# Kernel tuning notes

Hardware: AMD Instinct MI355X
Metric: run time of the kernel (lower is better)

## Reference

```python
import jax, jax.numpy as jnp
from jax import lax
import numpy as np

LEVELS = 5
KSIZE = 45
SIGMA0 = 1.0
SIZE_ADDER = 0
SIGMA_MULT = 2.0


def _gauss1d(ksize, sigma):
    # Matches cv2.getGaussianKernel for sigma > 0: normalized Gaussian samples.
    x = np.arange(ksize, dtype=np.float64) - (ksize - 1) / 2.0
    g = np.exp(-(x * x) / (2.0 * sigma * sigma))
    return g / g.sum()


def _gauss2d(ksize, sigma):
    g1 = _gauss1d(ksize, sigma)
    return jnp.asarray(np.outer(g1, g1), dtype=jnp.float32)  # (k, k)


_KERNELS = [_gauss2d(KSIZE + SIZE_ADDER, SIGMA0 * SIGMA_MULT ** lvl) for lvl in range(LEVELS)]


def _blur(img, k2d):
    """Depthwise 2D Gaussian blur with replicate padding. img: (N,C,H,W), k2d: (k,k)."""
    C = img.shape[1]
    k = k2d.shape[0]
    pad = k // 2
    imgp = jnp.pad(img, ((0, 0), (0, 0), (pad, pad), (pad, pad)), mode='edge')
    kern = jnp.broadcast_to(k2d.astype(img.dtype), (C, 1, k, k))  # same filter per channel
    return lax.conv_general_dilated(
        imgp, kern, window_strides=(1, 1), padding='VALID',
        dimension_numbers=('NCHW', 'OIHW', 'NCHW'), feature_group_count=C)


def _blend(img0, img1, mask):
    # Fused Laplacian-stack build for img0/img1, Gaussian-stack for mask, and
    # lerp + sum-over-levels accumulation in a single pass over levels.
    cur0, cur1, curm = img0, img1, mask
    acc = jnp.zeros_like(img0)
    for lvl in range(LEVELS):
        if lvl < LEVELS - 1:
            k2d = _KERNELS[lvl]
            b0 = _blur(cur0, k2d)
            b1 = _blur(cur1, k2d)
            bm = _blur(curm, k2d)
            lap0 = cur0 - b0
            lap1 = cur1 - b1
            acc = acc + lap0 + curm * (lap1 - lap0)  # lerp(lap0, lap1, gauss_mask)
            cur0, cur1, curm = b0, b1, bm
        else:
            acc = acc + cur0 + curm * (cur1 - cur0)
    return acc


def setup_inputs() -> dict:
    key = jax.random.key(0)
    k0, k1, k2 = jax.random.split(key, 3)
    img0 = jax.random.normal(k0, (16, 3, 512, 512), dtype=jnp.float32)
    img1 = jax.random.normal(k1, (16, 3, 512, 512), dtype=jnp.float32)
    mask = jax.random.uniform(k2, (16, 1, 512, 512), dtype=jnp.float32)
    return {"img0": img0, "img1": img1, "mask": mask}


def reference(img0, img1, mask):
    return _blend(img0, img1, mask)
```

## Files before the change

### kernel.cpp

```cpp
#include <hip/hip_runtime.h>

#define PH 512
#define PW 512
#define PLANE (PH * PW)
#define RS 68
#define PHYS(i) (((i) & 7) * 70 + ((i) >> 3))

enum { V_F0 = 0, V_MID = 1, V_L3D = 2, V_MONLY = 3 };

constexpr double cexp_pos(double z) {
  double term = 1.0, sum = 1.0;
  for (int k = 1; k < 160; ++k) {
    term *= z / (double)k;
    sum += term;
  }
  return sum;
}
template <int LVL, int R>
struct WTab {
  float w[2 * R + 1];
  constexpr WTab() : w{} {
    double sig = 1.0;
    for (int i = 0; i < LVL; ++i) sig *= 2.0;
    double g[2 * R + 1] = {};
    double s = 0.0;
    for (int t = 0; t <= 2 * R; ++t) {
      double x = (double)(t - R);
      g[t] = 1.0 / cexp_pos((x * x) / (2.0 * sig * sig));
      s += g[t];
    }
    for (int t = 0; t <= 2 * R; ++t) w[t] = (float)(g[t] / s);
  }
};

__device__ __forceinline__ int clampi(int v, int hi) {
  return v < 0 ? 0 : (v > hi ? hi : v);
}
__device__ __forceinline__ int swz(int bid, int nwg) {
  const int q = nwg >> 3;
  return (bid & 7) * q + (bid >> 3);
}
__device__ __forceinline__ float bf2f(ushort s) {
  return __uint_as_float((unsigned)s << 16);
}
__device__ __forceinline__ ushort f2bf(float f) {
  unsigned x = __float_as_uint(f);
  return (ushort)((x + 0x7FFF + ((x >> 16) & 1)) >> 16);
}
union BU { uint4 q; ushort u[8]; };
__device__ __forceinline__ void ldb8(const ushort* __restrict__ p, float* v) {
  BU b;
  b.q = *(const uint4*)p;
#pragma unroll
  for (int j = 0; j < 8; ++j) v[j] = bf2f(b.u[j]);
}
__device__ __forceinline__ void stb8(ushort* __restrict__ p, const float* v) {
  BU b;
#pragma unroll
  for (int j = 0; j < 8; ++j) b.u[j] = f2bf(v[j]);
  *(uint4*)p = b.q;
}
__device__ __forceinline__ void ldf8(const float* __restrict__ p, float* v) {
  float4 a = *(const float4*)p, b = *(const float4*)(p + 4);
  v[0] = a.x; v[1] = a.y; v[2] = a.z; v[3] = a.w;
  v[4] = b.x; v[5] = b.y; v[6] = b.z; v[7] = b.w;
}
__device__ __forceinline__ void stf8(float* __restrict__ p, const float* v) {
  *(float4*)p = make_float4(v[0], v[1], v[2], v[3]);
  *(float4*)(p + 4) = make_float4(v[4], v[5], v[6], v[7]);
}

template <int LVL, int R, bool LV0>
__global__ __launch_bounds__(256) void hpass_tele(
    const ushort* __restrict__ S, const float* __restrict__ in0,
    const float* __restrict__ in1, const float* __restrict__ inm,
    ushort* __restrict__ tmp, int cn3) {
  constexpr WTab<LVL, R> W;
  const int bid = swz(blockIdx.x, gridDim.x);
  const int tid = threadIdx.x;
  const int ry = tid >> 6, lr = tid & 63;
  const int p = bid >> 7;
  const int y = ((bid & 127) << 2) + ry;
  const int xb = lr << 3;

  __shared__ float lds[4][8 * 70];
  float* L = lds[ry];

  if (LV0) {
    if (p < cn3) {
      const float* rA = in0 + (size_t)p * PLANE + (size_t)y * PW;
      const float* rB = in1 + (size_t)p * PLANE + (size_t)y * PW;
      float a8[8], b8[8];
      ldf8(rA + xb, a8);
      ldf8(rB + xb, b8);
#pragma unroll
      for (int k = 0; k < 8; ++k) L[PHYS(R + xb + k)] = b8[k] - a8[k];
      if (lr < R) L[PHYS(lr)] = rB[0] - rA[0];
      else if (lr >= 32 && lr < 32 + R)
        L[PHYS(R + PW + (lr - 32))] = rB[PW - 1] - rA[PW - 1];
    } else {
      const float* rM = inm + (size_t)(p - cn3) * PLANE + (size_t)y * PW;
      float a8[8];
      ldf8(rM + xb, a8);
#pragma unroll
      for (int k = 0; k < 8; ++k) L[PHYS(R + xb + k)] = a8[k];
      if (lr < R) L[PHYS(lr)] = rM[0];
      else if (lr >= 32 && lr < 32 + R)
        L[PHYS(R + PW + (lr - 32))] = rM[PW - 1];
    }
  } else {
    const ushort* row = S + (size_t)p * PLANE + (size_t)y * PW;
    float a8[8];
    ldb8(row + xb, a8);
#pragma unroll
    for (int k = 0; k < 8; ++k) L[PHYS(R + xb + k)] = a8[k];
    if (lr < R) L[PHYS(lr)] = bf2f(row[0]);
    else if (lr >= 32 && lr < 32 + R)
      L[PHYS(R + PW + (lr - 32))] = bf2f(row[PW - 1]);
  }
  __syncthreads();

  float a[8];
#pragma unroll
  for (int i = 0; i < 8; ++i) a[i] = 0.f;
#pragma unroll
  for (int j = 0; j < 2 * R + 8; ++j) {
    const float v = L[PHYS(xb + j)];
#pragma unroll
    for (int i = 0; i < 8; ++i)
      if (i <= j && j - i <= 2 * R) a[i] = fmaf(W.w[j - i], v, a[i]);
  }
  stb8(tmp + (size_t)p * PLANE + (size_t)y * PW + xb, a);
}

template <int LVL, int R, int MODE>
__global__ __launch_bounds__(512) void vpass_tele(
    const ushort* __restrict__ tmp, const ushort* __restrict__ Sc,
    const ushort* __restrict__ Sm, const ushort* __restrict__ Gm4,
    const float* __restrict__ in0, const float* __restrict__ in1,
    const float* __restrict__ inm, ushort* __restrict__ oS,
    ushort* __restrict__ oM, float* __restrict__ outp, int cn3) {
  constexpr WTab<LVL, R> W;
  constexpr int VWIN = 64 + 2 * R;
  __shared__ float buf[VWIN * RS];
  const int bid = swz(blockIdx.x, gridDim.x);
  const int tid = threadIdx.x;
  const int lane = tid & 63, yg = tid >> 6;
  const int p = bid >> 6, t = bid & 63;
  const int x0 = (t & 7) << 6, y0 = (t >> 3) << 6;
  const int ey = tid >> 3, exq = (tid & 7) << 3;
  const size_t erow = (size_t)(y0 + ey) * PW + x0 + exq;

  const bool ismask = (MODE == V_MONLY) || (MODE != V_L3D && p >= cn3);
  const int pm = ismask ? ((MODE == V_MONLY) ? p : p - cn3) : 0;

  {
    const ushort* src = tmp + (size_t)(ismask ? (cn3 + pm) : p) * PLANE;
    for (int idx = tid; idx < VWIN * 8; idx += 512) {
      const int row = idx >> 3, c8 = (idx & 7) << 3;
      const int gy = clampi(y0 + row - R, PH - 1);
      BU b;
      b.q = *(const uint4*)&src[(size_t)gy * PW + x0 + c8];
      float* d = &buf[row * RS + c8];
#pragma unroll
      for (int j = 0; j < 8; ++j) d[j] = bf2f(b.u[j]);
    }
  }
  __syncthreads();

  float b[8];
#pragma unroll
  for (int i = 0; i < 8; ++i) b[i] = 0.f;
#pragma unroll
  for (int j = 0; j < 2 * R + 8; ++j) {
    const float v = buf[((yg << 3) + j) * RS + lane];
#pragma unroll
    for (int i = 0; i < 8; ++i)
      if (i <= j && j - i <= 2 * R) b[i] = fmaf(W.w[j - i], v, b[i]);
  }

  __syncthreads();
#pragma unroll
  for (int i = 0; i < 8; ++i) buf[lane * 65 + (yg << 3) + i] = b[i];
  __syncthreads();
  float bs[8];
#pragma unroll
  for (int j = 0; j < 8; ++j) bs[j] = buf[(exq + j) * 65 + ey];

  if (MODE == V_MONLY || ismask) {
    stb8(oM + (size_t)pm * PLANE + erow, bs);
    return;
  }

  const int n = p / 3;
  float o[8];
  if (MODE == V_F0) {
    float v0[8], v1[8], m[8];
    ldf8(in0 + (size_t)p * PLANE + erow, v0);
    ldf8(in1 + (size_t)p * PLANE + erow, v1);
    ldf8(inm + (size_t)n * PLANE + erow, m);
#pragma unroll
    for (int j = 0; j < 8; ++j)
      o[j] = v0[j] + m[j] * ((v1[j] - v0[j]) - bs[j]);
    stf8(outp + (size_t)p * PLANE + erow, o);
    stb8(oS + (size_t)p * PLANE + erow, bs);
  } else if (MODE == V_MID) {
    float D[8], m[8], pv[8];
    ldb8(Sc + (size_t)p * PLANE + erow, D);
    ldb8(Sm + (size_t)n * PLANE + erow, m);
    float* op = outp + (size_t)p * PLANE + erow;
    ldf8(op, pv);
#pragma unroll
    for (int j = 0; j < 8; ++j) o[j] = pv[j] + m[j] * (D[j] - bs[j]);
    stf8(op, o);
    stb8(oS + (size_t)p * PLANE + erow, bs);
  } else {
    float D[8], m3[8], m4[8], pv[8];
    ldb8(Sc + (size_t)p * PLANE + erow, D);
    ldb8(Sm + (size_t)n * PLANE + erow, m3);
    ldb8(Gm4 + (size_t)n * PLANE + erow, m4);
    float* op = outp + (size_t)p * PLANE + erow;
    ldf8(op, pv);
#pragma unroll
    for (int j = 0; j < 8; ++j)
      o[j] = pv[j] + m3[j] * (D[j] - bs[j]) + m4[j] * bs[j];
    stf8(op, o);
  }
}

extern "C" void kernel_launch(void* const* d_in, const int* in_sizes, int n_in,
                              void* d_out, int out_size, void* d_ws,
                              size_t ws_size, hipStream_t stream) {
  const float* img0 = (const float*)d_in[0];
  const float* img1 = (const float*)d_in[1];
  const float* mask = (const float*)d_in[2];
  float* out = (float*)d_out;

  constexpr int R0 = 6, R1 = 10, R2 = 18, R3v = 22;

  const int NTOT = 16;
  const size_t perImg = (size_t)12 * PLANE * sizeof(ushort);
  int CN = 16;
  while (CN > 1 && (size_t)CN * perImg > ws_size) CN >>= 1;

  for (int s = 0; s < NTOT; s += CN) {
    ushort* SA = (ushort*)d_ws;
    ushort* SB = SA + (size_t)4 * CN * PLANE;
    ushort* tmp = SB + (size_t)4 * CN * PLANE;

    const float* in0 = img0 + (size_t)s * 3 * PLANE;
    const float* in1 = img1 + (size_t)s * 3 * PLANE;
    const float* inm = mask + (size_t)s * PLANE;
    float* o = out + (size_t)s * 3 * PLANE;

    const int cn3 = 3 * CN;
    ushort* SAm = SA + (size_t)cn3 * PLANE;
    ushort* SBm = SB + (size_t)cn3 * PLANE;
    const ushort* nb = nullptr;
    const float* nf = nullptr;
    const dim3 hb(256), vb(512);
    const int hg = 4 * CN * 128;
    const int vg = 4 * CN * 64;
    const int vgM = CN * 64;
    const int vgD = 3 * CN * 64;

    hipLaunchKernelGGL((hpass_tele<0, R0, true>), dim3(hg), hb, 0, stream, nb,
                       in0, in1, inm, tmp, cn3);
    hipLaunchKernelGGL((vpass_tele<0, R0, V_F0>), dim3(vg), vb, 0, stream, tmp,
                       nb, nb, nb, in0, in1, inm, SA, SAm, o, cn3);
    hipLaunchKernelGGL((hpass_tele<1, R1, false>), dim3(hg), hb, 0, stream, SA,
                       nf, nf, nf, tmp, cn3);
    hipLaunchKernelGGL((vpass_tele<1, R1, V_MID>), dim3(vg), vb, 0, stream, tmp,
                       SA, SAm, nb, nf, nf, nf, SB, SBm, o, cn3);
    hipLaunchKernelGGL((hpass_tele<2, R2, false>), dim3(hg), hb, 0, stream, SB,
                       nf, nf, nf, tmp, cn3);
    hipLaunchKernelGGL((vpass_tele<2, R2, V_MID>), dim3(vg), vb, 0, stream, tmp,
                       SB, SBm, nb, nf, nf, nf, SA, SAm, o, cn3);
    hipLaunchKernelGGL((hpass_tele<3, R3v, false>), dim3(hg), hb, 0, stream, SA,
                       nf, nf, nf, tmp, cn3);
    hipLaunchKernelGGL((vpass_tele<3, R3v, V_MONLY>), dim3(vgM), vb, 0, stream,
                       tmp, nb, nb, nb, nf, nf, nf, (ushort*)nullptr, SBm, o,
                       cn3);
    hipLaunchKernelGGL((vpass_tele<3, R3v, V_L3D>), dim3(vgD), vb, 0, stream,
                       tmp, SA, SAm, SBm, nf, nf, nf, (ushort*)nullptr,
                       (ushort*)nullptr, o, cn3);
  }
}
```

Before: 240.7 us.

## Fuse horizontal and vertical blur passes per tile and store intermediates in fp16

Merges the separate horizontal-pass and vertical-pass kernels into one tiled kernel per level. Each block loads a haloed 2D window into LDS, runs the horizontal blur there, then the vertical blur, so the global tmp buffer round-trip goes away. Intermediate stacks and the running accumulator are now stored as fp16 instead of bf16 and fp32, which cuts traffic on the accumulator. In exchange, each block recomputes the horizontal blur on halo rows, uses more shared memory (which can lower occupancy at large radii), and fp16 has a narrower range than bf16.

```diff
diff --git a/kernel.cpp b/kernel.cpp
--- a/kernel.cpp
+++ b/kernel.cpp
@@ -3,10 +3,8 @@
 #define PH 512
 #define PW 512
 #define PLANE (PH * PW)
-#define RS 68
-#define PHYS(i) (((i) & 7) * 70 + ((i) >> 3))
-
-enum { V_F0 = 0, V_MID = 1, V_L3D = 2, V_MONLY = 3 };
+
+enum { M_F0 = 0, M_MID = 1, M_MONLY = 2, M_LAST = 3 };
 
 constexpr double cexp_pos(double z) {
   double term = 1.0, sum = 1.0;
@@ -40,28 +38,26 @@
   const int q = nwg >> 3;
   return (bid & 7) * q + (bid >> 3);
 }
-__device__ __forceinline__ float bf2f(ushort s) {
-  return __uint_as_float((unsigned)s << 16);
-}
-__device__ __forceinline__ ushort f2bf(float f) {
-  unsigned x = __float_as_uint(f);
-  return (ushort)((x + 0x7FFF + ((x >> 16) & 1)) >> 16);
-}
+union HU { ushort u; _Float16 h; };
 union BU { uint4 q; ushort u[8]; };
-__device__ __forceinline__ void ldb8(const ushort* __restrict__ p, float* v) {
+__device__ __forceinline__ float h2f(ushort s) {
+  HU x; x.u = s; return (float)x.h;
+}
+__device__ __forceinline__ ushort f2h(float f) {
+  HU x; x.h = (_Float16)f; return x.u;
+}
+__device__ __forceinline__ void q2f8(uint4 q, float* v) {
+  BU b; b.q = q;
+#pragma unroll
+  for (int j = 0; j < 8; ++j) v[j] = h2f(b.u[j]);
+}
+__device__ __forceinline__ void sth8(ushort* __restrict__ p, const float* v) {
   BU b;
-  b.q = *(const uint4*)p;
-#pragma unroll
-  for (int j = 0; j < 8; ++j) v[j] = bf2f(b.u[j]);
-}
-__device__ __forceinline__ void stb8(ushort* __restrict__ p, const float* v) {
-  BU b;
-#pragma unroll
-  for (int j = 0; j < 8; ++j) b.u[j] = f2bf(v[j]);
+#pragma unroll
+  for (int j = 0; j < 8; ++j) b.u[j] = f2h(v[j]);
   *(uint4*)p = b.q;
 }
-__device__ __forceinline__ void ldf8(const float* __restrict__ p, float* v) {
-  float4 a = *(const float4*)p, b = *(const float4*)(p + 4);
+__device__ __forceinline__ void ff2f8(float4 a, float4 b, float* v) {
   v[0] = a.x; v[1] = a.y; v[2] = a.z; v[3] = a.w;
   v[4] = b.x; v[5] = b.y; v[6] = b.z; v[7] = b.w;
 }
@@ -70,161 +66,199 @@
   *(float4*)(p + 4) = make_float4(v[4], v[5], v[6], v[7]);
 }
 
-template <int LVL, int R, bool LV0>
-__global__ __launch_bounds__(256) void hpass_tele(
-    const ushort* __restrict__ S, const float* __restrict__ in0,
+template <int LVL, int R, int MODE>
+__global__ __launch_bounds__(512) void fused_lvl(
+    const ushort* __restrict__ Sc, const ushort* __restrict__ Smk,
+    const ushort* __restrict__ Gm4p, const float* __restrict__ in0,
     const float* __restrict__ in1, const float* __restrict__ inm,
-    ushort* __restrict__ tmp, int cn3) {
-  constexpr WTab<LVL, R> W;
+    ushort* __restrict__ oS, ushort* __restrict__ oM,
+    ushort* __restrict__ accP, float* __restrict__ outp, int cn3) {
+  constexpr WTab<LVL, R> WT;
+  constexpr int R8 = ((R + 7) / 8) * 8;
+  constexpr int WW = 64 + 2 * R8;
+  constexpr int WSTR = WW + 6;
+  constexpr int VWIN = 64 + 2 * R;
+  constexpr int NCH = WW / 8;
+  __shared__ float Wb[VWIN * WSTR];
+  __shared__ float Hb[VWIN * 67];
+
   const int bid = swz(blockIdx.x, gridDim.x);
   const int tid = threadIdx.x;
-  const int ry = tid >> 6, lr = tid & 63;
-  const int p = bid >> 7;
-  const int y = ((bid & 127) << 2) + ry;
-  const int xb = lr << 3;
-
-  __shared__ float lds[4][8 * 70];
-  float* L = lds[ry];
-
-  if (LV0) {
-    if (p < cn3) {
-      const float* rA = in0 + (size_t)p * PLANE + (size_t)y * PW;
-      const float* rB = in1 + (size_t)p * PLANE + (size_t)y * PW;
-      float a8[8], b8[8];
-      ldf8(rA + xb, a8);
-      ldf8(rB + xb, b8);
-#pragma unroll
-      for (int k = 0; k < 8; ++k) L[PHYS(R + xb + k)] = b8[k] - a8[k];
-      if (lr < R) L[PHYS(lr)] = rB[0] - rA[0];
-      else if (lr >= 32 && lr < 32 + R)
-        L[PHYS(R + PW + (lr - 32))] = rB[PW - 1] - rA[PW - 1];
-    } else {
-      const float* rM = inm + (size_t)(p - cn3) * PLANE + (size_t)y * PW;
-      float a8[8];
-      ldf8(rM + xb, a8);
-#pragma unroll
-      for (int k = 0; k < 8; ++k) L[PHYS(R + xb + k)] = a8[k];
-      if (lr < R) L[PHYS(lr)] = rM[0];
-      else if (lr >= 32 && lr < 32 + R)
-        L[PHYS(R + PW + (lr - 32))] = rM[PW - 1];
-    }
-  } else {
-    const ushort* row = S + (size_t)p * PLANE + (size_t)y * PW;
-    float a8[8];
-    ldb8(row + xb, a8);
-#pragma unroll
-    for (int k = 0; k < 8; ++k) L[PHYS(R + xb + k)] = a8[k];
-    if (lr < R) L[PHYS(lr)] = bf2f(row[0]);
-    else if (lr >= 32 && lr < 32 + R)
-      L[PHYS(R + PW + (lr - 32))] = bf2f(row[PW - 1]);
-  }
-  __syncthreads();
-
-  float a[8];
-#pragma unroll
-  for (int i = 0; i < 8; ++i) a[i] = 0.f;
-#pragma unroll
-  for (int j = 0; j < 2 * R + 8; ++j) {
-    const float v = L[PHYS(xb + j)];
-#pragma unroll
-    for (int i = 0; i < 8; ++i)
-      if (i <= j && j - i <= 2 * R) a[i] = fmaf(W.w[j - i], v, a[i]);
-  }
-  stb8(tmp + (size_t)p * PLANE + (size_t)y * PW + xb, a);
-}
-
-template <int LVL, int R, int MODE>
-__global__ __launch_bounds__(512) void vpass_tele(
-    const ushort* __restrict__ tmp, const ushort* __restrict__ Sc,
-    const ushort* __restrict__ Sm, const ushort* __restrict__ Gm4,
-    const float* __restrict__ in0, const float* __restrict__ in1,
-    const float* __restrict__ inm, ushort* __restrict__ oS,
-    ushort* __restrict__ oM, float* __restrict__ outp, int cn3) {
-  constexpr WTab<LVL, R> W;
-  constexpr int VWIN = 64 + 2 * R;
-  __shared__ float buf[VWIN * RS];
-  const int bid = swz(blockIdx.x, gridDim.x);
-  const int tid = threadIdx.x;
-  const int lane = tid & 63, yg = tid >> 6;
   const int p = bid >> 6, t = bid & 63;
-  const int x0 = (t & 7) << 6, y0 = (t >> 3) << 6;
+  const int tx = t & 7;
+  const int x0 = tx << 6, y0 = (t >> 3) << 6;
+  const bool edge = (tx == 0) || (tx == 7);
   const int ey = tid >> 3, exq = (tid & 7) << 3;
   const size_t erow = (size_t)(y0 + ey) * PW + x0 + exq;
 
-  const bool ismask = (MODE == V_MONLY) || (MODE != V_L3D && p >= cn3);
-  const int pm = ismask ? ((MODE == V_MONLY) ? p : p - cn3) : 0;
+  const bool ismask = (MODE == M_MONLY) || (MODE != M_LAST && p >= cn3);
+  const int pm = ismask ? ((MODE == M_MONLY) ? p : p - cn3) : 0;
+  const int n = p / 3;
+
+  uint4 qacc{}, qm{}, qm4{};
+  float4 fi0a{}, fi0b{}, fmka{}, fmkb{};
+  if (!ismask) {
+    if (MODE == M_F0) {
+      const float* p0 = in0 + (size_t)p * PLANE + erow;
+      fi0a = ((const float4*)p0)[0];
+      fi0b = ((const float4*)p0)[1];
+      const float* pk = inm + (size_t)n * PLANE + erow;
+      fmka = ((const float4*)pk)[0];
+      fmkb = ((const float4*)pk)[1];
+    } else {
+      qacc = *(const uint4*)(accP + (size_t)p * PLANE + erow);
+      qm = *(const uint4*)(Smk + (size_t)n * PLANE + erow);
+      if (MODE == M_LAST)
+        qm4 = *(const uint4*)(Gm4p + (size_t)n * PLANE + erow);
+    }
+  }
 
   {
-    const ushort* src = tmp + (size_t)(ismask ? (cn3 + pm) : p) * PLANE;
-    for (int idx = tid; idx < VWIN * 8; idx += 512) {
-      const int row = idx >> 3, c8 = (idx & 7) << 3;
-      const int gy = clampi(y0 + row - R, PH - 1);
-      BU b;
-      b.q = *(const uint4*)&src[(size_t)gy * PW + x0 + c8];
-      float* d = &buf[row * RS + c8];
-#pragma unroll
-      for (int j = 0; j < 8; ++j) d[j] = bf2f(b.u[j]);
+    const int w = tid >> 6, rs = (tid >> 3) & 7, cs = tid & 7;
+#pragma unroll
+    for (int ro = 0; ro < VWIN; ro += 64) {
+      const int row = ro + (w << 3) + rs;
+#pragma unroll
+      for (int cb = 0; cb < 2; ++cb) {
+        const int ch = (cb << 3) + cs;
+        if (row < VWIN && ch < NCH) {
+          const int gy = clampi(y0 + row - R, PH - 1);
+          const int gx = x0 - R8 + (ch << 3);
+          float v[8];
+          if (MODE == M_F0) {
+            if (!ismask) {
+              const float* r0 = in0 + (size_t)p * PLANE + (size_t)gy * PW;
+              const float* r1 = in1 + (size_t)p * PLANE + (size_t)gy * PW;
+              if (!edge || (gx >= 0 && gx <= PW - 8)) {
+                float a[8], bb[8];
+                ff2f8(((const float4*)(r0 + gx))[0],
+                      ((const float4*)(r0 + gx))[1], a);
+                ff2f8(((const float4*)(r1 + gx))[0],
+                      ((const float4*)(r1 + gx))[1], bb);
+#pragma unroll
+                for (int j = 0; j < 8; ++j) v[j] = bb[j] - a[j];
+              } else {
+#pragma unroll
+                for (int j = 0; j < 8; ++j) {
+                  const int cx = clampi(gx + j, PW - 1);
+                  v[j] = r1[cx] - r0[cx];
+                }
+              }
+            } else {
+              const float* rm = inm + (size_t)pm * PLANE + (size_t)gy * PW;
+              if (!edge || (gx >= 0 && gx <= PW - 8)) {
+                ff2f8(((const float4*)(rm + gx))[0],
+                      ((const float4*)(rm + gx))[1], v);
+              } else {
+#pragma unroll
+                for (int j = 0; j < 8; ++j) v[j] = rm[clampi(gx + j, PW - 1)];
+              }
+            }
+          } else {
+            const ushort* sp =
+                (ismask ? Smk + (size_t)pm * PLANE : Sc + (size_t)p * PLANE) +
+                (size_t)gy * PW;
+            if (!edge || (gx >= 0 && gx <= PW - 8)) {
+              q2f8(*(const uint4*)&sp[gx], v);
+            } else {
+#pragma unroll
+              for (int j = 0; j < 8; ++j) v[j] = h2f(sp[clampi(gx + j, PW - 1)]);
+            }
+          }
+          float* d = &Wb[row * WSTR + (ch << 3)];
+#pragma unroll
+          for (int k = 0; k < 4; ++k)
+            *(float2*)&d[2 * k] = make_float2(v[2 * k], v[2 * k + 1]);
+        }
+      }
     }
   }
   __syncthreads();
 
+  {
+    const int cg = tid & 7;
+    constexpr int basep = R8 - R;
+#pragma unroll
+    for (int ro = 0; ro < VWIN; ro += 64) {
+      const int r = ro + (tid >> 3);
+      if (r < VWIN) {
+        const float* wr = &Wb[r * WSTR + basep + (cg << 3)];
+        float a[8];
+#pragma unroll
+        for (int i = 0; i < 8; ++i) a[i] = 0.f;
+#pragma unroll
+        for (int j2 = 0; j2 < R + 4; ++j2) {
+          const float2 v2 = *(const float2*)&wr[2 * j2];
+          const int j0 = 2 * j2, j1 = 2 * j2 + 1;
+#pragma unroll
+          for (int i = 0; i < 8; ++i) {
+            if (i <= j0 && j0 - i <= 2 * R)
+              a[i] = fmaf(WT.w[j0 - i], v2.x, a[i]);
+            if (i <= j1 && j1 - i <= 2 * R)
+              a[i] = fmaf(WT.w[j1 - i], v2.y, a[i]);
+          }
+        }
+        float* hr = &Hb[r * 67 + (cg << 3)];
+#pragma unroll
+        for (int i = 0; i < 8; ++i) hr[i] = a[i];
+      }
+    }
+  }
+  __syncthreads();
+
+  const int lane = tid & 63, yg = tid >> 6;
   float b[8];
 #pragma unroll
   for (int i = 0; i < 8; ++i) b[i] = 0.f;
 #pragma unroll
   for (int j = 0; j < 2 * R + 8; ++j) {
-    const float v = buf[((yg << 3) + j) * RS + lane];
+    const float v = Hb[((yg << 3) + j) * 67 + lane];
 #pragma unroll
     for (int i = 0; i < 8; ++i)
-      if (i <= j && j - i <= 2 * R) b[i] = fmaf(W.w[j - i], v, b[i]);
-  }
-
+      if (i <= j && j - i <= 2 * R) b[i] = fmaf(WT.w[j - i], v, b[i]);
+  }
   __syncthreads();
 #pragma unroll
-  for (int i = 0; i < 8; ++i) buf[lane * 65 + (yg << 3) + i] = b[i];
+  for (int i = 0; i < 8; ++i) Hb[lane * 65 + (yg << 3) + i] = b[i];
   __syncthreads();
   float bs[8];
 #pragma unroll
-  for (int j = 0; j < 8; ++j) bs[j] = buf[(exq + j) * 65 + ey];
-
-  if (MODE == V_MONLY || ismask) {
-    stb8(oM + (size_t)pm * PLANE + erow, bs);
+  for (int j = 0; j < 8; ++j) bs[j] = Hb[(exq + j) * 65 + ey];
+
+  if (ismask) {
+    sth8(oM + (size_t)pm * PLANE + erow, bs);
     return;
   }
 
-  const int n = p / 3;
-  float o[8];
-  if (MODE == V_F0) {
-    float v0[8], v1[8], m[8];
-    ldf8(in0 + (size_t)p * PLANE + erow, v0);
-    ldf8(in1 + (size_t)p * PLANE + erow, v1);
-    ldf8(inm + (size_t)n * PLANE + erow, m);
+  float D[8];
+#pragma unroll
+  for (int j = 0; j < 8; ++j) D[j] = Wb[(R + ey) * WSTR + R8 + exq + j];
+
+  if (MODE == M_F0) {
+    float i0v[8], mv[8], av[8];
+    ff2f8(fi0a, fi0b, i0v);
+    ff2f8(fmka, fmkb, mv);
+#pragma unroll
+    for (int j = 0; j < 8; ++j) av[j] = i0v[j] + mv[j] * (D[j] - bs[j]);
+    sth8(accP + (size_t)p * PLANE + erow, av);
+    sth8(oS + (size_t)p * PLANE + erow, bs);
+  } else if (MODE == M_MID) {
+    float av[8], mv[8];
+    q2f8(qacc, av);
+    q2f8(qm, mv);
+#pragma unroll
+    for (int j = 0; j < 8; ++j) av[j] += mv[j] * (D[j] - bs[j]);
+    sth8(accP + (size_t)p * PLANE + erow, av);
+    sth8(oS + (size_t)p * PLANE + erow, bs);
+  } else {
+    float av[8], m3[8], m4[8], o[8];
+    q2f8(qacc, av);
+    q2f8(qm, m3);
+    q2f8(qm4, m4);
 #pragma unroll
     for (int j = 0; j < 8; ++j)
-      o[j] = v0[j] + m[j] * ((v1[j] - v0[j]) - bs[j]);
+      o[j] = av[j] + m3[j] * (D[j] - bs[j]) + m4[j] * bs[j];
     stf8(outp + (size_t)p * PLANE + erow, o);
-    stb8(oS + (size_t)p * PLANE + erow, bs);
-  } else if (MODE == V_MID) {
-    float D[8], m[8], pv[8];
-    ldb8(Sc + (size_t)p * PLANE + erow, D);
-    ldb8(Sm + (size_t)n * PLANE + erow, m);
-    float* op = outp + (size_t)p * PLANE + erow;
-    ldf8(op, pv);
-#pragma unroll
-    for (int j = 0; j < 8; ++j) o[j] = pv[j] + m[j] * (D[j] - bs[j]);
-    stf8(op, o);
-    stb8(oS + (size_t)p * PLANE + erow, bs);
-  } else {
-    float D[8], m3[8], m4[8], pv[8];
-    ldb8(Sc + (size_t)p * PLANE + erow, D);
-    ldb8(Sm + (size_t)n * PLANE + erow, m3);
-    ldb8(Gm4 + (size_t)n * PLANE + erow, m4);
-    float* op = outp + (size_t)p * PLANE + erow;
-    ldf8(op, pv);
-#pragma unroll
-    for (int j = 0; j < 8; ++j)
-      o[j] = pv[j] + m3[j] * (D[j] - bs[j]) + m4[j] * bs[j];
-    stf8(op, o);
   }
 }
 
@@ -236,17 +270,17 @@
   const float* mask = (const float*)d_in[2];
   float* out = (float*)d_out;
 
-  constexpr int R0 = 6, R1 = 10, R2 = 18, R3v = 22;
-
   const int NTOT = 16;
-  const size_t perImg = (size_t)12 * PLANE * sizeof(ushort);
+  const size_t perImg = (size_t)11 * PLANE * sizeof(ushort);
   int CN = 16;
   while (CN > 1 && (size_t)CN * perImg > ws_size) CN >>= 1;
 
   for (int s = 0; s < NTOT; s += CN) {
     ushort* SA = (ushort*)d_ws;
     ushort* SB = SA + (size_t)4 * CN * PLANE;
-    ushort* tmp = SB + (size_t)4 * CN * PLANE;
+    ushort* acc = SB + (size_t)4 * CN * PLANE;
+    ushort* SAm = SA + (size_t)3 * CN * PLANE;
+    ushort* SBm = SB + (size_t)3 * CN * PLANE;
 
     const float* in0 = img0 + (size_t)s * 3 * PLANE;
     const float* in1 = img1 + (size_t)s * 3 * PLANE;
@@ -254,35 +288,25 @@
     float* o = out + (size_t)s * 3 * PLANE;
 
     const int cn3 = 3 * CN;
-    ushort* SAm = SA + (size_t)cn3 * PLANE;
-    ushort* SBm = SB + (size_t)cn3 * PLANE;
+    const dim3 blk(512);
+    const int gAll = 4 * CN * 64, gD = 3 * CN * 64, gM = CN * 64;
     const ushort* nb = nullptr;
     const float* nf = nullptr;
-    const dim3 hb(256), vb(512);
-    const int hg = 4 * CN * 128;
-    const int vg = 4 * CN * 64;
-    const int vgM = CN * 64;
-    const int vgD = 3 * CN * 64;
-
-    hipLaunchKernelGGL((hpass_tele<0, R0, true>), dim3(hg), hb, 0, stream, nb,
-                       in0, in1, inm, tmp, cn3);
-    hipLaunchKernelGGL((vpass_tele<0, R0, V_F0>), dim3(vg), vb, 0, stream, tmp,
-                       nb, nb, nb, in0, in1, inm, SA, SAm, o, cn3);
-    hipLaunchKernelGGL((hpass_tele<1, R1, false>), dim3(hg), hb, 0, stream, SA,
-                       nf, nf, nf, tmp, cn3);
-    hipLaunchKernelGGL((vpass_tele<1, R1, V_MID>), dim3(vg), vb, 0, stream, tmp,
-                       SA, SAm, nb, nf, nf, nf, SB, SBm, o, cn3);
-    hipLaunchKernelGGL((hpass_tele<2, R2, false>), dim3(hg), hb, 0, stream, SB,
-                       nf, nf, nf, tmp, cn3);
-    hipLaunchKernelGGL((vpass_tele<2, R2, V_MID>), dim3(vg), vb, 0, stream, tmp,
-                       SB, SBm, nb, nf, nf, nf, SA, SAm, o, cn3);
-    hipLaunchKernelGGL((hpass_tele<3, R3v, false>), dim3(hg), hb, 0, stream, SA,
-                       nf, nf, nf, tmp, cn3);
-    hipLaunchKernelGGL((vpass_tele<3, R3v, V_MONLY>), dim3(vgM), vb, 0, stream,
-                       tmp, nb, nb, nb, nf, nf, nf, (ushort*)nullptr, SBm, o,
+
+    hipLaunchKernelGGL((fused_lvl<0, 6, M_F0>), dim3(gAll), blk, 0, stream, nb,
+                       nb, nb, in0, in1, inm, SA, SAm, acc, (float*)nullptr,
                        cn3);
-    hipLaunchKernelGGL((vpass_tele<3, R3v, V_L3D>), dim3(vgD), vb, 0, stream,
-                       tmp, SA, SAm, SBm, nf, nf, nf, (ushort*)nullptr,
-                       (ushort*)nullptr, o, cn3);
-  }
-}
+    hipLaunchKernelGGL((fused_lvl<1, 10, M_MID>), dim3(gAll), blk, 0, stream,
+                       SA, SAm, nb, nf, nf, nf, SB, SBm, acc, (float*)nullptr,
+                       cn3);
+    hipLaunchKernelGGL((fused_lvl<2, 18, M_MID>), dim3(gAll), blk, 0, stream,
+                       SB, SBm, nb, nf, nf, nf, SA, SAm, acc, (float*)nullptr,
+                       cn3);
+    hipLaunchKernelGGL((fused_lvl<3, 22, M_MONLY>), dim3(gM), blk, 0, stream,
+                       nb, SAm, nb, nf, nf, nf, (ushort*)nullptr, SBm,
+                       (ushort*)nullptr, (float*)nullptr, cn3);
+    hipLaunchKernelGGL((fused_lvl<3, 22, M_LAST>), dim3(gD), blk, 0, stream, SA,
+                       SAm, SBm, nf, nf, nf, (ushort*)nullptr,
+                       (ushort*)nullptr, acc, o, cn3);
+  }
+}
```

New measurement: 239.7 us. Within noise of the previous version (-0.4%).
